# Performance work log

Measured on AMD Instinct MI355X. Metric: run time of the kernel, lower is better.

The kernel has to match this reference:

```python
import jax, jax.numpy as jnp
import numpy as np
from jax import lax

B, H, W = 4096, 15, 15
P, V = 16, 32
D = P + V            # 48
PCODE = 2380
NEMB = 2 * (PCODE + 1)  # 4762


def _conv(x, w, b=None, groups=1, pad='SAME'):
    # x: [B,C,H,W], w: [O, I/groups, kh, kw] (torch OIHW layout)
    y = lax.conv_general_dilated(
        x, w, window_strides=(1, 1), padding=pad,
        dimension_numbers=('NCHW', 'OIHW', 'NCHW'),
        feature_group_count=groups)
    if b is not None:
        y = y + b[None, :, None, None]
    return y


def setup_inputs() -> dict:
    key = jax.random.key(0)
    ks = jax.random.split(key, 18)
    f = lambda k, shape: (jax.random.normal(k, shape, jnp.float32) * 0.05)
    inp = {
        'emb': f(ks[0], (NEMB, D)),
        'conv_w': f(ks[1], (D, 1, 3, 3)),      # depthwise, groups=D
        'conv_b': f(ks[2], (D,)),
        'ppw_w': f(ks[3], (P, P, 1, 1)),
        'ppw_b': f(ks[4], (P,)),
        'pdw_w': f(ks[5], (P, 1, 3, 3)),       # depthwise, groups=P
        'pdw_b': f(ks[6], (P,)),
        'pf_w': f(ks[7], (1, P, 1, 1)),        # final policy conv, no bias
        'vpw_w': f(ks[8], (V, V, 1, 1)),
        'vpw_b': f(ks[9], (V,)),
        'vl1_w': f(ks[10], (V, V)),
        'vl1_b': f(ks[11], (V,)),
        'vl2_w': f(ks[12], (V, V)),
        'vl2_b': f(ks[13], (V,)),
        'vf_w': f(ks[14], (3, V)),
        'vf_b': f(ks[15], (3,)),
        'sparse_feature_input': jax.random.randint(ks[16], (B, 12, H, W), 0, PCODE, jnp.int32),
        'board_input': jax.random.randint(ks[17], (B, 2, H, W), 0, 2, jnp.int32),
    }
    return inp


def reference(emb, conv_w, conv_b, ppw_w, ppw_b, pdw_w, pdw_b, pf_w,
              vpw_w, vpw_b, vl1_w, vl1_b, vl2_w, vl2_b, vf_w, vf_b,
              sparse_feature_input, board_input):
    relu = jax.nn.relu
    # --- PatternCodeEmbedding ---
    pcode = sparse_feature_input[:, 10:12]                     # [B,2,H,W]
    pcode = jnp.where(board_input > 0, PCODE, pcode)
    pcode = pcode + jnp.array([0, PCODE + 1], jnp.int32)[None, :, None, None]
    feat = emb[pcode].sum(axis=1)                              # [B,H,W,D]
    feat = jnp.transpose(feat, (0, 3, 1, 2))                   # [B,D,H,W]
    # --- trunk depthwise conv ---
    feat = relu(_conv(feat, conv_w, conv_b, groups=D))
    # --- policy head ---
    pol = feat[:, :P]
    pol = relu(_conv(pol, ppw_w, ppw_b))
    pol = relu(_conv(pol, pdw_w, pdw_b, groups=P))
    pol = _conv(pol, pf_w)                                     # [B,1,H,W]
    # --- value head ---
    val = feat[:, P:]
    val = relu(_conv(val, vpw_w, vpw_b))
    val = jnp.mean(val, axis=(2, 3))                           # [B,V]
    val = relu(val @ vl1_w.T + vl1_b)
    val = relu(val @ vl2_w.T + vl2_b)
    val = val @ vf_w.T + vf_b                                  # [B,3]
    return val, pol
```

## Files before the change

### kernel.cpp

```cpp
#include <hip/hip_runtime.h>
#include <hip/hip_fp16.h>

typedef _Float16 half8  __attribute__((ext_vector_type(8)));
typedef _Float16 half4_t __attribute__((ext_vector_type(4)));
typedef _Float16 half2_t __attribute__((ext_vector_type(2)));
typedef __fp16   fp16x2  __attribute__((ext_vector_type(2)));
typedef float f32x4 __attribute__((ext_vector_type(4)));

namespace {
constexpr int NT = 256;
constexpr int NPIX = 225;
constexpr int PCODE_C = 2380;

constexpr int APITCH_Y  = 272;
constexpr int APITCH_CG = 4624;

constexpr int OFF_A     = 0;
constexpr int OFF_X     = 27744;
constexpr int OFF_WC    = 50784;
constexpr int OFF_WCB   = 51648;
constexpr int OFF_WPD   = 51744;
constexpr int OFF_WPDB  = 52032;
constexpr int OFF_SV    = 52064;
constexpr int OFF_H1    = 52192;
constexpr int OFF_H2    = 52320;
constexpr int SMEM_BYTES = 52448;

constexpr int OFF_POLA  = 0;
}

__device__ __forceinline__ half2_t pkrtz(float a, float b) {
    return __builtin_bit_cast(half2_t, __builtin_amdgcn_cvt_pkrtz(a, b));
}
__device__ __forceinline__ void wave_fence() {
    asm volatile("s_waitcnt lgkmcnt(0)" ::: "memory");
}

__global__ __launch_bounds__(NT, 3) void patnet_kernel(
    const float* __restrict__ emb,
    const float* __restrict__ conv_w, const float* __restrict__ conv_b,
    const float* __restrict__ ppw_w,  const float* __restrict__ ppw_b,
    const float* __restrict__ pdw_w,  const float* __restrict__ pdw_b,
    const float* __restrict__ pf_w,
    const float* __restrict__ vpw_w,  const float* __restrict__ vpw_b,
    const float* __restrict__ vl1_w,  const float* __restrict__ vl1_b,
    const float* __restrict__ vl2_w,  const float* __restrict__ vl2_b,
    const float* __restrict__ vf_w,   const float* __restrict__ vf_b,
    const int* __restrict__ sparse,   const int* __restrict__ board,
    float* __restrict__ out, int batch)
{
    __shared__ __align__(16) unsigned char smem[SMEM_BYTES];
    const int tid  = threadIdx.x;
    const int b    = blockIdx.x;
    const int lane = tid & 63;
    const int wave = tid >> 6;

    int c0 = 0, c1 = 0;
    if (tid < NPIX) {
        int s10 = sparse[b * 2700 + 10 * NPIX + tid];
        int s11 = sparse[b * 2700 + 11 * NPIX + tid];
        int b0  = board[b * 450 + tid];
        int b1  = board[b * 450 + NPIX + tid];
        c0 = (b0 > 0) ? PCODE_C : s10;
        c1 = ((b1 > 0) ? PCODE_C : s11) + (PCODE_C + 1);
    }

    {
        _Float16* Wc   = (_Float16*)(smem + OFF_WC);
        _Float16* Wcb  = (_Float16*)(smem + OFF_WCB);
        _Float16* Wpd  = (_Float16*)(smem + OFF_WPD);
        _Float16* Wpdb = (_Float16*)(smem + OFF_WPDB);
        for (int i = tid; i < 432; i += NT) {
            int cg = i / 72, rem = i - cg * 72;
            int t = rem >> 3, j = rem & 7;
            Wc[i] = (_Float16)conv_w[(cg * 8 + j) * 9 + t];
        }
        for (int i = tid; i < 48; i += NT) Wcb[i] = (_Float16)conv_b[i];
        for (int i = tid; i < 144; i += NT) {
            int cg = i / 72, rem = i - cg * 72;
            int t = rem >> 3, j = rem & 7;
            Wpd[i] = (_Float16)pdw_w[(cg * 8 + j) * 9 + t];
        }
        for (int i = tid; i < 16; i += NT) Wpdb[i] = (_Float16)pdw_b[i];
        for (int i = tid; i < 384; i += NT) {
            int cg = i >> 6, j = i & 63;
            int row, col;
            if (j < 17)      { row = 0;  col = j; }
            else if (j < 34) { row = 16; col = j - 17; }
            else { int k = j - 34; row = 1 + (k >> 1); col = (k & 1) * 16; }
            *(half8*)(smem + OFF_A + cg * APITCH_CG + row * APITCH_Y + col * 16) = (half8)(_Float16)0.f;
        }
    }

    if (tid < NPIX) {
        const float* e0 = emb + c0 * 48;
        const float* e1 = emb + c1 * 48;
        int y = tid / 15, x = tid - y * 15;
        unsigned char* abase = smem + OFF_A + (y + 1) * APITCH_Y + (x + 1) * 16;
        #pragma unroll
        for (int g = 0; g < 6; g++) {
            f32x4 x0 = *(const f32x4*)(e0 + g * 8);
            f32x4 x1 = *(const f32x4*)(e0 + g * 8 + 4);
            f32x4 y0 = *(const f32x4*)(e1 + g * 8);
            f32x4 y1 = *(const f32x4*)(e1 + g * 8 + 4);
            f32x4 s0 = x0 + y0, s1 = x1 + y1;
            half2_t q0 = pkrtz(s0.x, s0.y), q1 = pkrtz(s0.z, s0.w);
            half2_t q2 = pkrtz(s1.x, s1.y), q3 = pkrtz(s1.z, s1.w);
            half8 hv = {q0[0], q0[1], q1[0], q1[1], q2[0], q2[1], q3[0], q3[1]};
            *(half8*)(abase + g * APITCH_CG) = hv;
        }
    }
    __syncthreads();

    auto do_strip = [&](int t) {
        int cg = t / 45, rem = t - cg * 45;
        int y = rem / 3, s = rem - y * 3;
        int xs = s * 5;
        const unsigned char* wb = smem + OFF_WC + cg * 144;
        half8 wv[9];
        #pragma unroll
        for (int i = 0; i < 9; i++) wv[i] = *(const half8*)(wb + i * 16);
        half8 bias = *(const half8*)(smem + OFF_WCB + cg * 16);
        half8 acc[5] = {bias, bias, bias, bias, bias};
        const unsigned char* ab = smem + OFF_A + cg * APITCH_CG + y * APITCH_Y + xs * 16;
        #pragma unroll
        for (int c = 0; c < 7; c++) {
            half8 v0 = *(const half8*)(ab + c * 16);
            half8 v1 = *(const half8*)(ab + APITCH_Y + c * 16);
            half8 v2 = *(const half8*)(ab + 2 * APITCH_Y + c * 16);
            #pragma unroll
            for (int o = 0; o < 5; o++) {
                int kx = c - o;
                if (kx >= 0 && kx <= 2) {
                    acc[o] = __builtin_elementwise_fma(v0, wv[kx],     acc[o]);
                    acc[o] = __builtin_elementwise_fma(v1, wv[3 + kx], acc[o]);
                    acc[o] = __builtin_elementwise_fma(v2, wv[6 + kx], acc[o]);
                }
            }
        }
        unsigned char* xw = smem + OFF_X + (y * 15 + xs) * 96 + cg * 16;
        #pragma unroll
        for (int o = 0; o < 5; o++)
            *(half8*)(xw + o * 96) = __builtin_elementwise_max(acc[o], (half8)(_Float16)0.f);
    };
    do_strip(tid);
    {
        int e = wave * 4 + lane;
        if (lane < 4 && e < 14) do_strip(256 + e);
    }

    const int n = lane & 15, q = lane >> 4;
    half8 af_p;
    {
        const float* wp = ppw_w + n * 16 + (q & 1) * 8;
        f32x4 w0 = *(const f32x4*)wp, w1 = *(const f32x4*)(wp + 4);
        half8 t = {(_Float16)w0.x, (_Float16)w0.y, (_Float16)w0.z, (_Float16)w0.w,
                   (_Float16)w1.x, (_Float16)w1.y, (_Float16)w1.z, (_Float16)w1.w};
        af_p = (q < 2) ? t : (half8)(_Float16)0.f;
    }
    f32x4 pb = *(const f32x4*)(ppw_b + q * 4);
    half2_t pfh[8];
    #pragma unroll
    for (int j = 0; j < 8; j++) pfh[j] = pkrtz(pf_w[2 * j], pf_w[2 * j + 1]);
    half8 af0, af1;
    {
        const float* wp = vpw_w + n * 32 + q * 8;
        f32x4 w0 = *(const f32x4*)wp, w1 = *(const f32x4*)(wp + 4);
        af0 = half8{(_Float16)w0.x, (_Float16)w0.y, (_Float16)w0.z, (_Float16)w0.w,
                    (_Float16)w1.x, (_Float16)w1.y, (_Float16)w1.z, (_Float16)w1.w};
        const float* wp2 = vpw_w + (16 + n) * 32 + q * 8;
        f32x4 v0 = *(const f32x4*)wp2, v1 = *(const f32x4*)(wp2 + 4);
        af1 = half8{(_Float16)v0.x, (_Float16)v0.y, (_Float16)v0.z, (_Float16)v0.w,
                    (_Float16)v1.x, (_Float16)v1.y, (_Float16)v1.z, (_Float16)v1.w};
    }
    f32x4 vb0 = *(const f32x4*)(vpw_b + q * 4);
    f32x4 vb1 = *(const f32x4*)(vpw_b + 16 + q * 4);
    __syncthreads();

    if (wave < 3) {
        #pragma unroll
        for (int i0 = 0; i0 < 2; i0++) {
            int i = i0 * 64 + lane;
            int cg = i >> 6, j = i & 63;
            int row, col;
            if (j < 17)      { row = 0;  col = j; }
            else if (j < 34) { row = 16; col = j - 17; }
            else { int k = j - 34; row = 1 + (k >> 1); col = (k & 1) * 16; }
            *(half8*)(smem + OFF_POLA + cg * APITCH_CG + row * APITCH_Y + col * 16) = (half8)(_Float16)0.f;
        }
        const int cgp = lane & 1;
        half8 wvp[9];
        #pragma unroll
        for (int t = 0; t < 9; t++) wvp[t] = *(const half8*)(smem + OFF_WPD + cgp * 144 + t * 16);
        half8 biasp = *(const half8*)(smem + OFF_WPDB + cgp * 16);

        const int tlo = (wave == 0) ? 0 : ((wave == 1) ? 3 : 8);
        const int thi = (wave == 0) ? 6 : ((wave == 1) ? 11 : 15);
        const int cg3 = q >> 1;
        for (int t = tlo; t < thi; t++) {
            int p = t * 16 + n;
            half8 bf = *(const half8*)(smem + OFF_X + p * 96 + q * 16);
            f32x4 d = __builtin_amdgcn_mfma_f32_16x16x32_f16(af_p, bf, (f32x4)(0.f), 0, 0, 0);
            if (p < NPIX) {
                int y = p / 15, x = p - y * 15;
                half2_t lo = pkrtz(fmaxf(d.x + pb.x, 0.f), fmaxf(d.y + pb.y, 0.f));
                half2_t hi = pkrtz(fmaxf(d.z + pb.z, 0.f), fmaxf(d.w + pb.w, 0.f));
                half4_t hv = {lo[0], lo[1], hi[0], hi[1]};
                *(half4_t*)(smem + OFF_POLA + cg3 * APITCH_CG + (y + 1) * APITCH_Y + (x + 1) * 16 + (q & 1) * 8) = hv;
            }
        }
        wave_fence();

        const int px0 = wave * 75;
        for (int i = 0; i < 3; i++) {
            int idx = i * 64 + lane;
            if (idx < 150) {
                int px = px0 + (idx >> 1);
                int y = px / 15, x = px - y * 15;
                const unsigned char* pbse = smem + OFF_POLA + cgp * APITCH_CG + y * APITCH_Y + x * 16;
                half8 acc = biasp;
                #pragma unroll
                for (int ky = 0; ky < 3; ky++) {
                    acc = __builtin_elementwise_fma(*(const half8*)(pbse + ky * APITCH_Y),      wvp[ky * 3 + 0], acc);
                    acc = __builtin_elementwise_fma(*(const half8*)(pbse + ky * APITCH_Y + 16), wvp[ky * 3 + 1], acc);
                    acc = __builtin_elementwise_fma(*(const half8*)(pbse + ky * APITCH_Y + 32), wvp[ky * 3 + 2], acc);
                }
                acc = __builtin_elementwise_max(acc, (half8)(_Float16)0.f);
                float part = 0.f;
                part = __builtin_amdgcn_fdot2(half2_t{acc[0], acc[1]}, pfh[cgp * 4 + 0], part, false);
                part = __builtin_amdgcn_fdot2(half2_t{acc[2], acc[3]}, pfh[cgp * 4 + 1], part, false);
                part = __builtin_amdgcn_fdot2(half2_t{acc[4], acc[5]}, pfh[cgp * 4 + 2], part, false);
                part = __builtin_amdgcn_fdot2(half2_t{acc[6], acc[7]}, pfh[cgp * 4 + 3], part, false);
                float tot = part + __shfl_xor(part, 1, 64);
                if (cgp == 0) out[3 * batch + b * NPIX + px] = tot;
            }
        }
    } else {
        f32x4 a0 = {0.f, 0.f, 0.f, 0.f}, a1 = {0.f, 0.f, 0.f, 0.f};
        for (int t = 0; t < 15; t++) {
            int p = t * 16 + n;
            half8 bf = *(const half8*)(smem + OFF_X + p * 96 + 32 + q * 16);
            f32x4 d0 = __builtin_amdgcn_mfma_f32_16x16x32_f16(af0, bf, (f32x4)(0.f), 0, 0, 0);
            f32x4 d1 = __builtin_amdgcn_mfma_f32_16x16x32_f16(af1, bf, (f32x4)(0.f), 0, 0, 0);
            if (p < NPIX) {
                #pragma unroll
                for (int r = 0; r < 4; r++) {
                    a0[r] += fmaxf(d0[r] + vb0[r], 0.f);
                    a1[r] += fmaxf(d1[r] + vb1[r], 0.f);
                }
            }
        }
        #pragma unroll
        for (int s = 1; s < 16; s <<= 1) {
            #pragma unroll
            for (int r = 0; r < 4; r++) {
                a0[r] += __shfl_xor(a0[r], s, 64);
                a1[r] += __shfl_xor(a1[r], s, 64);
            }
        }
        if (n == 0) {
            *(f32x4*)(smem + OFF_SV + q * 16)      = a0 * (1.f / 225.f);
            *(f32x4*)(smem + OFF_SV + 64 + q * 16) = a1 * (1.f / 225.f);
        }
        const int o = lane & 31;
        f32x4 w1r[8], w2r[8], w3r[8];
        float b1v = vl1_b[o], b2v = vl2_b[o], b3v = 0.f;
        #pragma unroll
        for (int g = 0; g < 8; g++) w1r[g] = *(const f32x4*)(vl1_w + o * 32 + g * 4);
        #pragma unroll
        for (int g = 0; g < 8; g++) w2r[g] = *(const f32x4*)(vl2_w + o * 32 + g * 4);
        if (lane < 3) {
            b3v = vf_b[lane];
            #pragma unroll
            for (int g = 0; g < 8; g++) w3r[g] = *(const f32x4*)(vf_w + lane * 32 + g * 4);
        }
        wave_fence();

        float acc1 = b1v;
        #pragma unroll
        for (int g = 0; g < 8; g++) {
            f32x4 sv = *(const f32x4*)(smem + OFF_SV + g * 16);
            acc1 += sv.x * w1r[g].x + sv.y * w1r[g].y + sv.z * w1r[g].z + sv.w * w1r[g].w;
        }
        acc1 = fmaxf(acc1, 0.f);
        if (lane < 32) *(float*)(smem + OFF_H1 + o * 4) = acc1;
        wave_fence();

        float acc2 = b2v;
        #pragma unroll
        for (int g = 0; g < 8; g++) {
            f32x4 hv = *(const f32x4*)(smem + OFF_H1 + g * 16);
            acc2 += hv.x * w2r[g].x + hv.y * w2r[g].y + hv.z * w2r[g].z + hv.w * w2r[g].w;
        }
        acc2 = fmaxf(acc2, 0.f);
        if (lane < 32) *(float*)(smem + OFF_H2 + o * 4) = acc2;
        wave_fence();

        if (lane < 3) {
            float acc3 = b3v;
            #pragma unroll
            for (int g = 0; g < 8; g++) {
                f32x4 hv = *(const f32x4*)(smem + OFF_H2 + g * 16);
                acc3 += hv.x * w3r[g].x + hv.y * w3r[g].y + hv.z * w3r[g].z + hv.w * w3r[g].w;
            }
            out[b * 3 + lane] = acc3;
        }
    }
}

extern "C" void kernel_launch(void* const* d_in, const int* in_sizes, int n_in,
                              void* d_out, int out_size, void* d_ws, size_t ws_size,
                              hipStream_t stream) {
    const float* emb    = (const float*)d_in[0];
    const float* conv_w = (const float*)d_in[1];
    const float* conv_b = (const float*)d_in[2];
    const float* ppw_w  = (const float*)d_in[3];
    const float* ppw_b  = (const float*)d_in[4];
    const float* pdw_w  = (const float*)d_in[5];
    const float* pdw_b  = (const float*)d_in[6];
    const float* pf_w   = (const float*)d_in[7];
    const float* vpw_w  = (const float*)d_in[8];
    const float* vpw_b  = (const float*)d_in[9];
    const float* vl1_w  = (const float*)d_in[10];
    const float* vl1_b  = (const float*)d_in[11];
    const float* vl2_w  = (const float*)d_in[12];
    const float* vl2_b  = (const float*)d_in[13];
    const float* vf_w   = (const float*)d_in[14];
    const float* vf_b   = (const float*)d_in[15];
    const int* sparse   = (const int*)d_in[16];
    const int* board    = (const int*)d_in[17];
    float* out = (float*)d_out;

    int batch = in_sizes[16] / 2700;
    patnet_kernel<<<batch, NT, 0, stream>>>(
        emb, conv_w, conv_b, ppw_w, ppw_b, pdw_w, pdw_b, pf_w,
        vpw_w, vpw_b, vl1_w, vl1_b, vl2_w, vl2_b, vf_w, vf_b,
        sparse, board, out, batch);
}
```

Measured before the change: 174.4 us.

## Alias conv output over input buffer in LDS to raise occupancy to four blocks

The depthwise conv now computes all strips into registers, synchronises, and then writes its output into the region that held the padded input. This shrinks shared memory from about 52KB to about 38KB, and the launch bound goes from 3 to 4 blocks per CU. The feature row pitch changes from 96 to 112 bytes, likely to reduce LDS bank conflicts on the MFMA B-operand loads. Zeroing of the policy padding buffer moves before the barrier, since that buffer no longer aliases the input. In exchange, the kernel adds one barrier, keeps both accumulator sets live in registers across it, and faces a tighter register budget at 4 blocks per CU.

```diff
diff --git a/kernel.cpp b/kernel.cpp
--- a/kernel.cpp
+++ b/kernel.cpp
@@ -4,7 +4,6 @@
 typedef _Float16 half8  __attribute__((ext_vector_type(8)));
 typedef _Float16 half4_t __attribute__((ext_vector_type(4)));
 typedef _Float16 half2_t __attribute__((ext_vector_type(2)));
-typedef __fp16   fp16x2  __attribute__((ext_vector_type(2)));
 typedef float f32x4 __attribute__((ext_vector_type(4)));
 
 namespace {
@@ -14,19 +13,19 @@
 
 constexpr int APITCH_Y  = 272;
 constexpr int APITCH_CG = 4624;
+constexpr int XPITCH = 112;
 
 constexpr int OFF_A     = 0;
-constexpr int OFF_X     = 27744;
-constexpr int OFF_WC    = 50784;
-constexpr int OFF_WCB   = 51648;
-constexpr int OFF_WPD   = 51744;
-constexpr int OFF_WPDB  = 52032;
-constexpr int OFF_SV    = 52064;
-constexpr int OFF_H1    = 52192;
-constexpr int OFF_H2    = 52320;
-constexpr int SMEM_BYTES = 52448;
-
-constexpr int OFF_POLA  = 0;
+constexpr int OFF_X     = 0;
+constexpr int OFF_POLA  = 26880;
+constexpr int OFF_WC    = 36128;
+constexpr int OFF_WCB   = 36992;
+constexpr int OFF_WPD   = 37088;
+constexpr int OFF_WPDB  = 37376;
+constexpr int OFF_SV    = 37408;
+constexpr int OFF_H1    = 37536;
+constexpr int OFF_H2    = 37664;
+constexpr int SMEM_BYTES = 37792;
 }
 
 __device__ __forceinline__ half2_t pkrtz(float a, float b) {
@@ -36,7 +35,7 @@
     asm volatile("s_waitcnt lgkmcnt(0)" ::: "memory");
 }
 
-__global__ __launch_bounds__(NT, 3) void patnet_kernel(
+__global__ __launch_bounds__(NT, 4) void patnet_kernel(
     const float* __restrict__ emb,
     const float* __restrict__ conv_w, const float* __restrict__ conv_b,
     const float* __restrict__ ppw_w,  const float* __restrict__ ppw_b,
@@ -112,7 +111,7 @@
     }
     __syncthreads();
 
-    auto do_strip = [&](int t) {
+    auto compute_strip = [&](int t, half8* acc) {
         int cg = t / 45, rem = t - cg * 45;
         int y = rem / 3, s = rem - y * 3;
         int xs = s * 5;
@@ -121,7 +120,8 @@
         #pragma unroll
         for (int i = 0; i < 9; i++) wv[i] = *(const half8*)(wb + i * 16);
         half8 bias = *(const half8*)(smem + OFF_WCB + cg * 16);
-        half8 acc[5] = {bias, bias, bias, bias, bias};
+        #pragma unroll
+        for (int o = 0; o < 5; o++) acc[o] = bias;
         const unsigned char* ab = smem + OFF_A + cg * APITCH_CG + y * APITCH_Y + xs * 16;
         #pragma unroll
         for (int c = 0; c < 7; c++) {
@@ -138,15 +138,34 @@
                 }
             }
         }
-        unsigned char* xw = smem + OFF_X + (y * 15 + xs) * 96 + cg * 16;
+    };
+    auto write_strip = [&](int t, half8* acc) {
+        int cg = t / 45, rem = t - cg * 45;
+        int y = rem / 3, s = rem - y * 3;
+        int xs = s * 5;
+        unsigned char* xw = smem + OFF_X + (y * 15 + xs) * XPITCH + cg * 16;
         #pragma unroll
         for (int o = 0; o < 5; o++)
-            *(half8*)(xw + o * 96) = __builtin_elementwise_max(acc[o], (half8)(_Float16)0.f);
+            *(half8*)(xw + o * XPITCH) = __builtin_elementwise_max(acc[o], (half8)(_Float16)0.f);
     };
-    do_strip(tid);
-    {
-        int e = wave * 4 + lane;
-        if (lane < 4 && e < 14) do_strip(256 + e);
+
+    half8 acc1[5];
+    compute_strip(tid, acc1);
+    const int e = wave * 4 + lane;
+    const bool has2 = (lane < 4) && (e < 14);
+    half8 acc2[5];
+    if (has2) compute_strip(256 + e, acc2);
+    __syncthreads();
+
+    write_strip(tid, acc1);
+    if (has2) write_strip(256 + e, acc2);
+    if (tid < 128) {
+        int cg = tid >> 6, j = tid & 63;
+        int row, col;
+        if (j < 17)      { row = 0;  col = j; }
+        else if (j < 34) { row = 16; col = j - 17; }
+        else { int k = j - 34; row = 1 + (k >> 1); col = (k & 1) * 16; }
+        *(half8*)(smem + OFF_POLA + cg * APITCH_CG + row * APITCH_Y + col * 16) = (half8)(_Float16)0.f;
     }
 
     const int n = lane & 15, q = lane >> 4;
@@ -178,16 +197,6 @@
     __syncthreads();
 
     if (wave < 3) {
-        #pragma unroll
-        for (int i0 = 0; i0 < 2; i0++) {
-            int i = i0 * 64 + lane;
-            int cg = i >> 6, j = i & 63;
-            int row, col;
-            if (j < 17)      { row = 0;  col = j; }
-            else if (j < 34) { row = 16; col = j - 17; }
-            else { int k = j - 34; row = 1 + (k >> 1); col = (k & 1) * 16; }
-            *(half8*)(smem + OFF_POLA + cg * APITCH_CG + row * APITCH_Y + col * 16) = (half8)(_Float16)0.f;
-        }
         const int cgp = lane & 1;
         half8 wvp[9];
         #pragma unroll
@@ -199,7 +208,7 @@
         const int cg3 = q >> 1;
         for (int t = tlo; t < thi; t++) {
             int p = t * 16 + n;
-            half8 bf = *(const half8*)(smem + OFF_X + p * 96 + q * 16);
+            half8 bf = *(const half8*)(smem + OFF_X + p * XPITCH + q * 16);
             f32x4 d = __builtin_amdgcn_mfma_f32_16x16x32_f16(af_p, bf, (f32x4)(0.f), 0, 0, 0);
             if (p < NPIX) {
                 int y = p / 15, x = p - y * 15;
@@ -239,7 +248,7 @@
         f32x4 a0 = {0.f, 0.f, 0.f, 0.f}, a1 = {0.f, 0.f, 0.f, 0.f};
         for (int t = 0; t < 15; t++) {
             int p = t * 16 + n;
-            half8 bf = *(const half8*)(smem + OFF_X + p * 96 + 32 + q * 16);
+            half8 bf = *(const half8*)(smem + OFF_X + p * XPITCH + 32 + q * 16);
             f32x4 d0 = __builtin_amdgcn_mfma_f32_16x16x32_f16(af0, bf, (f32x4)(0.f), 0, 0, 0);
             f32x4 d1 = __builtin_amdgcn_mfma_f32_16x16x32_f16(af1, bf, (f32x4)(0.f), 0, 0, 0);
             if (p < NPIX) {
@@ -276,34 +285,34 @@
         }
         wave_fence();
 
-        float acc1 = b1v;
+        float acc1f = b1v;
         #pragma unroll
         for (int g = 0; g < 8; g++) {
             f32x4 sv = *(const f32x4*)(smem + OFF_SV + g * 16);
-            acc1 += sv.x * w1r[g].x + sv.y * w1r[g].y + sv.z * w1r[g].z + sv.w * w1r[g].w;
-        }
-        acc1 = fmaxf(acc1, 0.f);
-        if (lane < 32) *(float*)(smem + OFF_H1 + o * 4) = acc1;
+            acc1f += sv.x * w1r[g].x + sv.y * w1r[g].y + sv.z * w1r[g].z + sv.w * w1r[g].w;
+        }
+        acc1f = fmaxf(acc1f, 0.f);
+        if (lane < 32) *(float*)(smem + OFF_H1 + o * 4) = acc1f;
         wave_fence();
 
-        float acc2 = b2v;
+        float acc2f = b2v;
         #pragma unroll
         for (int g = 0; g < 8; g++) {
             f32x4 hv = *(const f32x4*)(smem + OFF_H1 + g * 16);
-            acc2 += hv.x * w2r[g].x + hv.y * w2r[g].y + hv.z * w2r[g].z + hv.w * w2r[g].w;
-        }
-        acc2 = fmaxf(acc2, 0.f);
-        if (lane < 32) *(float*)(smem + OFF_H2 + o * 4) = acc2;
+            acc2f += hv.x * w2r[g].x + hv.y * w2r[g].y + hv.z * w2r[g].z + hv.w * w2r[g].w;
+        }
+        acc2f = fmaxf(acc2f, 0.f);
+        if (lane < 32) *(float*)(smem + OFF_H2 + o * 4) = acc2f;
         wave_fence();
 
         if (lane < 3) {
-            float acc3 = b3v;
+            float acc3f = b3v;
             #pragma unroll
             for (int g = 0; g < 8; g++) {
                 f32x4 hv = *(const f32x4*)(smem + OFF_H2 + g * 16);
-                acc3 += hv.x * w3r[g].x + hv.y * w3r[g].y + hv.z * w3r[g].z + hv.w * w3r[g].w;
-            }
-            out[b * 3 + lane] = acc3;
+                acc3f += hv.x * w3r[g].x + hv.y * w3r[g].y + hv.z * w3r[g].z + hv.w * w3r[g].w;
+            }
+            out[b * 3 + lane] = acc3f;
         }
     }
 }
```

Result: slower. 237.5 us (+36.2%).
